# Optimization experiments

Hardware: AMD Instinct MI355X
Metric: run time of the kernel (lower is better)

## Reference

```python
import jax, jax.numpy as jnp
import numpy as np

N = 100000
E = 600000
NODE_DIM = 128
EDGE_DIM = 32
HIDDEN = 128  # must equal NODE_DIM (index_add_ into zeros_like(node_features))


def _linear_params(key, fan_in, fan_out):
    kw, kb = jax.random.split(key)
    bound = 1.0 / np.sqrt(fan_in)
    W = jax.random.uniform(kw, (fan_in, fan_out), minval=-bound, maxval=bound, dtype=jnp.float32)
    b = jax.random.uniform(kb, (fan_out,), minval=-bound, maxval=bound, dtype=jnp.float32)
    return W, b


def setup_inputs() -> dict:
    key = jax.random.key(0)
    ks = jax.random.split(key, 8)
    node_features = jax.random.normal(ks[0], (N, NODE_DIM), dtype=jnp.float32)
    edge_index = jax.random.randint(ks[1], (2, E), 0, N, dtype=jnp.int32)
    edge_features = jax.random.normal(ks[2], (E, EDGE_DIM), dtype=jnp.float32)
    m_W1, m_b1 = _linear_params(ks[3], 2 * NODE_DIM + EDGE_DIM, HIDDEN)
    m_W2, m_b2 = _linear_params(ks[4], HIDDEN, HIDDEN)
    a_W, a_b = _linear_params(ks[5], HIDDEN, 1)
    u_W1, u_b1 = _linear_params(ks[6], NODE_DIM + HIDDEN, HIDDEN)
    u_W2, u_b2 = _linear_params(ks[7], HIDDEN, NODE_DIM)
    return {
        "node_features": node_features,
        "edge_features": edge_features,
        "m_W1": m_W1, "m_b1": m_b1, "m_W2": m_W2, "m_b2": m_b2,
        "a_W": a_W, "a_b": a_b,
        "u_W1": u_W1, "u_b1": u_b1, "u_W2": u_W2, "u_b2": u_b2,
        "edge_index": edge_index,
    }


def reference(node_features, edge_features, m_W1, m_b1, m_W2, m_b2,
              a_W, a_b, u_W1, u_b1, u_W2, u_b2, edge_index):
    row, col = edge_index[0], edge_index[1]
    # gather endpoints + edge feats -> [E, 2*node_dim + edge_dim]
    msg_in = jnp.concatenate([node_features[row], node_features[col], edge_features], axis=-1)
    # message MLP
    h = jax.nn.relu(msg_in @ m_W1 + m_b1)
    messages = h @ m_W2 + m_b2  # [E, hidden]
    # global softmax over all edges (dim=0), per attention column (width 1)
    attn = jax.nn.softmax(messages @ a_W + a_b, axis=0)  # [E, 1]
    messages = messages * attn
    # scatter-add into destination nodes
    aggregated = jax.ops.segment_sum(messages, col, num_segments=node_features.shape[0])
    # update MLP + residual
    upd_in = jnp.concatenate([node_features, aggregated], axis=-1)
    u = jax.nn.relu(upd_in @ u_W1 + u_b1)
    updated = u @ u_W2 + u_b2
    return updated + node_features
```

## Files before the change

### kernel.cpp

```cpp
#include <hip/hip_runtime.h>
#include <hip/hip_bf16.h>
#include <stdint.h>

#define NN 100000
#define NE 600000
#define ND 128
#define ED 32
#define HID 128
#define SCANB 391

using short8 = __attribute__((ext_vector_type(8))) short;
using f32x4  = __attribute__((ext_vector_type(4))) float;

__device__ __forceinline__ uint32_t f2bf(float f) {
  uint32_t u = __float_as_uint(f);
  return (u + 0x7FFFu + ((u >> 16) & 1u)) >> 16;
}
__device__ __forceinline__ short8 pack8(float4 a, float4 b) {
  short8 s;
  s[0] = (short)f2bf(a.x); s[1] = (short)f2bf(a.y);
  s[2] = (short)f2bf(a.z); s[3] = (short)f2bf(a.w);
  s[4] = (short)f2bf(b.x); s[5] = (short)f2bf(b.y);
  s[6] = (short)f2bf(b.z); s[7] = (short)f2bf(b.w);
  return s;
}

__global__ __launch_bounds__(256) void k_prep(
    const float* __restrict__ W1, const float* __restrict__ W2,
    const float* __restrict__ uW1, const float* __restrict__ uW2,
    short* __restrict__ W1p, short* __restrict__ W2p,
    short* __restrict__ U1p, short* __restrict__ U2p) {
  int o = blockIdx.x * 256 + threadIdx.x;
  const float* src; short* dst; int rel;
  if (o < 36864)      { rel = o;         src = W1;  dst = W1p; }
  else if (o < 53248) { rel = o - 36864; src = W2;  dst = W2p; }
  else if (o < 86016) { rel = o - 53248; src = uW1; dst = U1p; }
  else                { rel = o - 86016; src = uW2; dst = U2p; }
  int j = rel & 7, c16 = (rel >> 3) & 15, g = (rel >> 7) & 3, nt = (rel >> 9) & 7, c = rel >> 12;
  int k = c * 32 + g * 8 + j, n = nt * 16 + c16;
  dst[rel] = (short)f2bf(src[k * 128 + n]);
}

__global__ __launch_bounds__(256) void k_prep_nf(const float* __restrict__ nf,
                                                 short* __restrict__ nfb) {
  const int total = NN * ND / 8;
  for (int u = blockIdx.x * 256 + threadIdx.x; u < total; u += gridDim.x * 256) {
    const float* s = nf + (size_t)u * 8;
    float4 v0 = *(const float4*)s, v1 = *(const float4*)(s + 4);
    *(short8*)(nfb + (size_t)u * 8) = pack8(v0, v1);
  }
}

__global__ __launch_bounds__(256, 2) void k_edge_mfma(
    const short* __restrict__ nfb, const float* __restrict__ ef,
    const short* __restrict__ W1p, const float* __restrict__ b1,
    const short* __restrict__ W2p, const float* __restrict__ b2,
    const float* __restrict__ aW, const int* __restrict__ ei,
    const int* __restrict__ perm,
    uint16_t* __restrict__ msg, float* __restrict__ logits) {
  __shared__ __align__(16) short sA[192 * 40];
  __shared__ __align__(16) short sB[4096];
  __shared__ __align__(16) short sH[192 * 136];
  __shared__ int sIdx[384];
  __shared__ int sPerm[192];

  const int tid = threadIdx.x;
  const int wv = tid >> 6, ln = tid & 63, cr = ln & 15, gp = ln >> 4;
  const int e0 = blockIdx.x * 192;
  const int wrow = wv * 48;

  if (tid < 192) {
    sIdx[tid] = ei[e0 + tid];
    sIdx[192 + tid] = ei[NE + e0 + tid];
    sPerm[tid] = perm[e0 + tid];
  }

  float bia[8], aWr[8], bia2[8];
#pragma unroll
  for (int nt = 0; nt < 8; ++nt) {
    bia[nt] = b1[nt * 16 + cr];
    bia2[nt] = b2[nt * 16 + cr];
    aWr[nt] = aW[nt * 16 + cr];
  }
  f32x4 acc[3][8];
#pragma unroll
  for (int mt = 0; mt < 3; ++mt)
#pragma unroll
    for (int nt = 0; nt < 8; ++nt)
      acc[mt][nt] = (f32x4){bia[nt], bia[nt], bia[nt], bia[nt]};
  __syncthreads();

  for (int c = 0; c < 9; ++c) {
#pragma unroll
    for (int it = 0; it < 3; ++it) {
      int row = it * 64 + (tid >> 2), k8 = (tid & 3) * 8;
      if (c < 8) {
        const short* src = nfb + (size_t)sIdx[(c < 4 ? 0 : 192) + row] * ND +
                           (c & 3) * 32 + k8;
        *(short8*)&sA[row * 40 + k8] = *(const short8*)src;
      } else {
        const float* src = ef + (size_t)(e0 + row) * ED + k8;
        float4 v0 = *(const float4*)src, v1 = *(const float4*)(src + 4);
        *(short8*)&sA[row * 40 + k8] = pack8(v0, v1);
      }
    }
    {
      const short8* wsrc = (const short8*)(W1p + c * 4096);
      short8 t0 = wsrc[tid], t1 = wsrc[tid + 256];
      ((short8*)sB)[tid] = t0; ((short8*)sB)[tid + 256] = t1;
    }
    __syncthreads();
    short8 af[3];
#pragma unroll
    for (int mt = 0; mt < 3; ++mt)
      af[mt] = *(const short8*)&sA[(wrow + mt * 16 + cr) * 40 + gp * 8];
#pragma unroll
    for (int nt = 0; nt < 8; ++nt) {
      short8 bfr = *(const short8*)&sB[(nt * 4 + gp) * 128 + cr * 8];
#pragma unroll
      for (int mt = 0; mt < 3; ++mt)
        acc[mt][nt] = __builtin_amdgcn_mfma_f32_16x16x32_bf16(af[mt], bfr, acc[mt][nt], 0, 0, 0);
    }
    __syncthreads();
  }

#pragma unroll
  for (int mt = 0; mt < 3; ++mt)
#pragma unroll
    for (int nt = 0; nt < 8; ++nt)
#pragma unroll
      for (int rr = 0; rr < 4; ++rr)
        sH[(wrow + mt * 16 + gp * 4 + rr) * 136 + nt * 16 + cr] =
            (short)f2bf(fmaxf(acc[mt][nt][rr], 0.f));
  __syncthreads();

  f32x4 acc2[3][8];
#pragma unroll
  for (int mt = 0; mt < 3; ++mt)
#pragma unroll
    for (int nt = 0; nt < 8; ++nt)
      acc2[mt][nt] = (f32x4){bia2[nt], bia2[nt], bia2[nt], bia2[nt]};
  for (int c2 = 0; c2 < 4; ++c2) {
    {
      const short8* wsrc = (const short8*)(W2p + c2 * 4096);
      short8 t0 = wsrc[tid], t1 = wsrc[tid + 256];
      ((short8*)sB)[tid] = t0; ((short8*)sB)[tid + 256] = t1;
    }
    __syncthreads();
    short8 af[3];
#pragma unroll
    for (int mt = 0; mt < 3; ++mt)
      af[mt] = *(const short8*)&sH[(wrow + mt * 16 + cr) * 136 + c2 * 32 + gp * 8];
#pragma unroll
    for (int nt = 0; nt < 8; ++nt) {
      short8 bfr = *(const short8*)&sB[(nt * 4 + gp) * 128 + cr * 8];
#pragma unroll
      for (int mt = 0; mt < 3; ++mt)
        acc2[mt][nt] = __builtin_amdgcn_mfma_f32_16x16x32_bf16(af[mt], bfr, acc2[mt][nt], 0, 0, 0);
    }
    __syncthreads();
  }

#pragma unroll
  for (int mt = 0; mt < 3; ++mt)
#pragma unroll
    for (int rr = 0; rr < 4; ++rr) {
      float p = 0.f;
#pragma unroll
      for (int nt = 0; nt < 8; ++nt) p += acc2[mt][nt][rr] * aWr[nt];
      p += __shfl_xor(p, 1, 64);
      p += __shfl_xor(p, 2, 64);
      p += __shfl_xor(p, 4, 64);
      p += __shfl_xor(p, 8, 64);
      if (cr == 0) logits[sPerm[wrow + mt * 16 + gp * 4 + rr]] = p;
    }

#pragma unroll
  for (int mt = 0; mt < 3; ++mt)
#pragma unroll
    for (int nt = 0; nt < 8; ++nt)
#pragma unroll
      for (int rr = 0; rr < 4; ++rr)
        sH[(wrow + mt * 16 + gp * 4 + rr) * 136 + nt * 16 + cr] =
            (short)f2bf(acc2[mt][nt][rr]);
  __syncthreads();
#pragma unroll
  for (int it = 0; it < 12; ++it) {
    int row = it * 16 + (tid >> 4), o8 = (tid & 15) * 8;
    *(short8*)(msg + (size_t)sPerm[row] * HID + o8) = *(const short8*)&sH[row * 136 + o8];
  }
}

__global__ __launch_bounds__(256, 2) void k_node_mfma(
    const float* __restrict__ nf, const short* __restrict__ nfb,
    const float* __restrict__ agg,
    const short* __restrict__ U1p, const float* __restrict__ b1,
    const short* __restrict__ U2p, const float* __restrict__ b2,
    float* __restrict__ out) {
  __shared__ __align__(16) short sA[192 * 40];
  __shared__ __align__(16) short sB[4096];
  __shared__ __align__(16) short sH[192 * 136];

  const int tid = threadIdx.x;
  const int wv = tid >> 6, ln = tid & 63, cr = ln & 15, gp = ln >> 4;
  const int n0 = blockIdx.x * 192;
  const int wrow = wv * 48;

  float bia[8], bia2[8];
#pragma unroll
  for (int nt = 0; nt < 8; ++nt) {
    bia[nt] = b1[nt * 16 + cr];
    bia2[nt] = b2[nt * 16 + cr];
  }
  f32x4 acc[3][8];
#pragma unroll
  for (int mt = 0; mt < 3; ++mt)
#pragma unroll
    for (int nt = 0; nt < 8; ++nt)
      acc[mt][nt] = (f32x4){bia[nt], bia[nt], bia[nt], bia[nt]};

  for (int c = 0; c < 8; ++c) {
#pragma unroll
    for (int it = 0; it < 3; ++it) {
      int row = it * 64 + (tid >> 2), k8 = (tid & 3) * 8;
      int n = n0 + row; if (n >= NN) n = NN - 1;
      if (c < 4) {
        *(short8*)&sA[row * 40 + k8] =
            *(const short8*)(nfb + (size_t)n * ND + c * 32 + k8);
      } else {
        const float* src = agg + (size_t)n * ND + (c - 4) * 32 + k8;
        float4 v0 = *(const float4*)src, v1 = *(const float4*)(src + 4);
        *(short8*)&sA[row * 40 + k8] = pack8(v0, v1);
      }
    }
    {
      const short8* wsrc = (const short8*)(U1p + c * 4096);
      short8 t0 = wsrc[tid], t1 = wsrc[tid + 256];
      ((short8*)sB)[tid] = t0; ((short8*)sB)[tid + 256] = t1;
    }
    __syncthreads();
    short8 af[3];
#pragma unroll
    for (int mt = 0; mt < 3; ++mt)
      af[mt] = *(const short8*)&sA[(wrow + mt * 16 + cr) * 40 + gp * 8];
#pragma unroll
    for (int nt = 0; nt < 8; ++nt) {
      short8 bfr = *(const short8*)&sB[(nt * 4 + gp) * 128 + cr * 8];
#pragma unroll
      for (int mt = 0; mt < 3; ++mt)
        acc[mt][nt] = __builtin_amdgcn_mfma_f32_16x16x32_bf16(af[mt], bfr, acc[mt][nt], 0, 0, 0);
    }
    __syncthreads();
  }

#pragma unroll
  for (int mt = 0; mt < 3; ++mt)
#pragma unroll
    for (int nt = 0; nt < 8; ++nt)
#pragma unroll
      for (int rr = 0; rr < 4; ++rr)
        sH[(wrow + mt * 16 + gp * 4 + rr) * 136 + nt * 16 + cr] =
            (short)f2bf(fmaxf(acc[mt][nt][rr], 0.f));
  __syncthreads();

  f32x4 acc2[3][8];
#pragma unroll
  for (int mt = 0; mt < 3; ++mt)
#pragma unroll
    for (int nt = 0; nt < 8; ++nt)
      acc2[mt][nt] = (f32x4){bia2[nt], bia2[nt], bia2[nt], bia2[nt]};
  for (int c2 = 0; c2 < 4; ++c2) {
    {
      const short8* wsrc = (const short8*)(U2p + c2 * 4096);
      short8 t0 = wsrc[tid], t1 = wsrc[tid + 256];
      ((short8*)sB)[tid] = t0; ((short8*)sB)[tid + 256] = t1;
    }
    __syncthreads();
    short8 af[3];
#pragma unroll
    for (int mt = 0; mt < 3; ++mt)
      af[mt] = *(const short8*)&sH[(wrow + mt * 16 + cr) * 136 + c2 * 32 + gp * 8];
#pragma unroll
    for (int nt = 0; nt < 8; ++nt) {
      short8 bfr = *(const short8*)&sB[(nt * 4 + gp) * 128 + cr * 8];
#pragma unroll
      for (int mt = 0; mt < 3; ++mt)
        acc2[mt][nt] = __builtin_amdgcn_mfma_f32_16x16x32_bf16(af[mt], bfr, acc2[mt][nt], 0, 0, 0);
    }
    __syncthreads();
  }

#pragma unroll
  for (int mt = 0; mt < 3; ++mt)
#pragma unroll
    for (int rr = 0; rr < 4; ++rr) {
      int n = n0 + wrow + mt * 16 + gp * 4 + rr;
      if (n < NN) {
#pragma unroll
        for (int nt = 0; nt < 8; ++nt) {
          int col = nt * 16 + cr;
          out[(size_t)n * ND + col] = acc2[mt][nt][rr] + nf[(size_t)n * ND + col];
        }
      }
    }
}

__device__ __forceinline__ void ms_combine(float& m, float& s, float m2, float s2) {
  float M = fmaxf(m, m2);
  s = s * expf(m - M) + s2 * expf(m2 - M);
  m = M;
}
__device__ __forceinline__ void ms_block_reduce(float& m, float& s) {
#pragma unroll
  for (int o = 1; o < 64; o <<= 1) {
    float m2 = __shfl_xor(m, o, 64), s2 = __shfl_xor(s, o, 64);
    ms_combine(m, s, m2, s2);
  }
  __shared__ float sm[4], ss[4];
  if ((threadIdx.x & 63) == 0) { sm[threadIdx.x >> 6] = m; ss[threadIdx.x >> 6] = s; }
  __syncthreads();
  m = sm[0]; s = ss[0];
  ms_combine(m, s, sm[1], ss[1]);
  ms_combine(m, s, sm[2], ss[2]);
  ms_combine(m, s, sm[3], ss[3]);
}
__global__ __launch_bounds__(256) void k_red_p(const float* __restrict__ logits,
                                               float* __restrict__ pmax,
                                               float* __restrict__ psum) {
  float m = -3.402823466e38f, s = 0.f;
  for (int i = blockIdx.x * 256 + threadIdx.x; i < NE; i += 1024 * 256) {
    float l = logits[i];
    if (l <= m) s += expf(l - m);
    else { s = s * expf(m - l) + 1.f; m = l; }
  }
  ms_block_reduce(m, s);
  if (threadIdx.x == 0) { pmax[blockIdx.x] = m; psum[blockIdx.x] = s; }
}
__global__ __launch_bounds__(256) void k_red_f(const float* __restrict__ pmax,
                                               const float* __restrict__ psum,
                                               float* __restrict__ red) {
  float m = pmax[threadIdx.x], s = psum[threadIdx.x];
  ms_combine(m, s, pmax[threadIdx.x + 256], psum[threadIdx.x + 256]);
  ms_combine(m, s, pmax[threadIdx.x + 512], psum[threadIdx.x + 512]);
  ms_combine(m, s, pmax[threadIdx.x + 768], psum[threadIdx.x + 768]);
  ms_block_reduce(m, s);
  if (threadIdx.x == 0) { red[0] = m; red[1] = 1.0f / s; }
}

__global__ __launch_bounds__(256) void k_zero_cnt(int* __restrict__ cnt) {
  int i = blockIdx.x * 256 + threadIdx.x;
  if (i < NN) cnt[i] = 0;
}
__global__ __launch_bounds__(256) void k_hist(const int* __restrict__ ei,
                                              int* __restrict__ cnt) {
  int e = blockIdx.x * 256 + threadIdx.x;
  if (e < NE) atomicAdd(&cnt[ei[NE + e]], 1);
}
__global__ __launch_bounds__(256) void k_scan_bsum(const int* __restrict__ cnt,
                                                   int* __restrict__ bsum) {
  int i = blockIdx.x * 256 + threadIdx.x;
  int v = (i < NN) ? cnt[i] : 0;
#pragma unroll
  for (int s = 1; s < 64; s <<= 1) v += __shfl_xor(v, s, 64);
  __shared__ int sv[4];
  if ((threadIdx.x & 63) == 0) sv[threadIdx.x >> 6] = v;
  __syncthreads();
  if (threadIdx.x == 0) bsum[blockIdx.x] = sv[0] + sv[1] + sv[2] + sv[3];
}
__global__ __launch_bounds__(512) void k_scan_boff(const int* __restrict__ bsum,
                                                   int* __restrict__ boff,
                                                   int* __restrict__ rowptr) {
  __shared__ int s[512];
  int t = threadIdx.x;
  int v = (t < SCANB) ? bsum[t] : 0;
  s[t] = v;
  __syncthreads();
  for (int off = 1; off < 512; off <<= 1) {
    int u = (t >= off) ? s[t - off] : 0;
    __syncthreads();
    s[t] += u;
    __syncthreads();
  }
  if (t < SCANB) boff[t] = s[t] - v;
  if (t == 0) rowptr[NN] = NE;
}
__global__ __launch_bounds__(256) void k_scan_final(int* __restrict__ cnt,
                                                    const int* __restrict__ boff,
                                                    int* __restrict__ rowptr) {
  __shared__ int s[256];
  int b = blockIdx.x, t = threadIdx.x, i = b * 256 + t;
  int v = (i < NN) ? cnt[i] : 0;
  s[t] = v;
  __syncthreads();
  for (int off = 1; off < 256; off <<= 1) {
    int u = (t >= off) ? s[t - off] : 0;
    __syncthreads();
    s[t] += u;
    __syncthreads();
  }
  int excl = s[t] - v + boff[b];
  if (i < NN) { rowptr[i] = excl; cnt[i] = excl; }
}
__global__ __launch_bounds__(256) void k_fill(const int* __restrict__ ei,
                                              int* __restrict__ cursor,
                                              int* __restrict__ perm) {
  int e = blockIdx.x * 256 + threadIdx.x;
  if (e >= NE) return;
  int c = ei[NE + e];
  int pos = atomicAdd(&cursor[c], 1);
  perm[e] = pos;
}

__global__ __launch_bounds__(256) void k_agg(
    const uint16_t* __restrict__ msg, const float* __restrict__ logits,
    const int* __restrict__ rowptr, const float* __restrict__ red,
    float* __restrict__ out) {
  int n = blockIdx.x * 4 + (threadIdx.x >> 6);
  int lane = threadIdx.x & 63;
  if (n >= NN) return;
  float gm = red[0], inv = red[1];
  int i0 = rowptr[n], i1 = rowptr[n + 1];
  float a0 = 0.f, a1 = 0.f;
  for (int i = i0; i < i1; ++i) {
    float wt = expf(logits[i] - gm) * inv;
    uint32_t pk = *(const uint32_t*)(msg + (size_t)i * HID + lane * 2);
    a0 += wt * __uint_as_float(pk << 16);
    a1 += wt * __uint_as_float(pk & 0xFFFF0000u);
  }
  *(float2*)(out + (size_t)n * ND + lane * 2) = make_float2(a0, a1);
}

extern "C" void kernel_launch(void* const* d_in, const int* in_sizes, int n_in,
                              void* d_out, int out_size, void* d_ws, size_t ws_size,
                              hipStream_t stream) {
  const float* nf  = (const float*)d_in[0];
  const float* ef  = (const float*)d_in[1];
  const float* mW1 = (const float*)d_in[2];
  const float* mb1 = (const float*)d_in[3];
  const float* mW2 = (const float*)d_in[4];
  const float* mb2 = (const float*)d_in[5];
  const float* aW  = (const float*)d_in[6];
  const float* uW1 = (const float*)d_in[8];
  const float* ub1 = (const float*)d_in[9];
  const float* uW2 = (const float*)d_in[10];
  const float* ub2 = (const float*)d_in[11];
  const int*   ei  = (const int*)d_in[12];
  float* out = (float*)d_out;

  char* ws = (char*)d_ws;
  uint16_t* msg = (uint16_t*)ws;
  float* logits = (float*)(ws + 153600000);
  float* pmax = (float*)(ws + 156000000);
  float* psum = pmax + 1024;
  float* red  = psum + 1024;
  short* W1p = (short*)(ws + 156008256);
  short* W2p = W1p + 36864;
  short* U1p = W2p + 16384;
  short* U2p = U1p + 32768;
  int* rowptr = (int*)(ws + 156213056);
  int* cnt    = rowptr + (NN + 1);
  int* perm   = cnt + NN;
  int* bsum   = perm + NE;
  int* boff   = bsum + 512;
  short* nfb  = (short*)(ws + 159420416);

  k_prep<<<400, 256, 0, stream>>>(mW1, mW2, uW1, uW2, W1p, W2p, U1p, U2p);
  k_prep_nf<<<2048, 256, 0, stream>>>(nf, nfb);
  k_zero_cnt<<<SCANB, 256, 0, stream>>>(cnt);
  k_hist<<<(NE + 255) / 256, 256, 0, stream>>>(ei, cnt);
  k_scan_bsum<<<SCANB, 256, 0, stream>>>(cnt, bsum);
  k_scan_boff<<<1, 512, 0, stream>>>(bsum, boff, rowptr);
  k_scan_final<<<SCANB, 256, 0, stream>>>(cnt, boff, rowptr);
  k_fill<<<(NE + 255) / 256, 256, 0, stream>>>(ei, cnt, perm);
  k_edge_mfma<<<NE / 192, 256, 0, stream>>>(nfb, ef, W1p, mb1, W2p, mb2, aW, ei, perm, msg, logits);
  k_red_p<<<1024, 256, 0, stream>>>(logits, pmax, psum);
  k_red_f<<<1, 256, 0, stream>>>(pmax, psum, red);
  k_agg<<<(NN + 3) / 4, 256, 0, stream>>>(msg, logits, rowptr, red, out);
  k_node_mfma<<<(NN + 191) / 192, 256, 0, stream>>>(nf, nfb, out, U1p, ub1, U2p, ub2, out);
}
```

Baseline: 361.6 us.

## Process edges in sorted order and fuse softmax partial reduction into edge kernel

Result: slower. 386.4 us (+6.9%).

```diff
diff --git a/kernel.cpp b/kernel.cpp
--- a/kernel.cpp
+++ b/kernel.cpp
@@ -8,6 +8,7 @@
 #define ED 32
 #define HID 128
 #define SCANB 391
+#define NB (NE / 192)
 
 using short8 = __attribute__((ext_vector_type(8))) short;
 using f32x4  = __attribute__((ext_vector_type(4))) float;
@@ -23,6 +24,26 @@
   s[4] = (short)f2bf(b.x); s[5] = (short)f2bf(b.y);
   s[6] = (short)f2bf(b.z); s[7] = (short)f2bf(b.w);
   return s;
+}
+
+__device__ __forceinline__ void ms_combine(float& m, float& s, float m2, float s2) {
+  float M = fmaxf(m, m2);
+  s = s * expf(m - M) + s2 * expf(m2 - M);
+  m = M;
+}
+__device__ __forceinline__ void ms_block_reduce(float& m, float& s) {
+#pragma unroll
+  for (int o = 1; o < 64; o <<= 1) {
+    float m2 = __shfl_xor(m, o, 64), s2 = __shfl_xor(s, o, 64);
+    ms_combine(m, s, m2, s2);
+  }
+  __shared__ float sm[4], ss[4];
+  if ((threadIdx.x & 63) == 0) { sm[threadIdx.x >> 6] = m; ss[threadIdx.x >> 6] = s; }
+  __syncthreads();
+  m = sm[0]; s = ss[0];
+  ms_combine(m, s, sm[1], ss[1]);
+  ms_combine(m, s, sm[2], ss[2]);
+  ms_combine(m, s, sm[3], ss[3]);
 }
 
 __global__ __launch_bounds__(256) void k_prep(
@@ -56,13 +77,14 @@
     const short* __restrict__ W1p, const float* __restrict__ b1,
     const short* __restrict__ W2p, const float* __restrict__ b2,
     const float* __restrict__ aW, const int* __restrict__ ei,
-    const int* __restrict__ perm,
-    uint16_t* __restrict__ msg, float* __restrict__ logits) {
+    const int* __restrict__ eid,
+    uint16_t* __restrict__ msg, float* __restrict__ logits,
+    float* __restrict__ pmaxp, float* __restrict__ psump) {
   __shared__ __align__(16) short sA[192 * 40];
   __shared__ __align__(16) short sB[4096];
   __shared__ __align__(16) short sH[192 * 136];
   __shared__ int sIdx[384];
-  __shared__ int sPerm[192];
+  __shared__ int sEid[192];
 
   const int tid = threadIdx.x;
   const int wv = tid >> 6, ln = tid & 63, cr = ln & 15, gp = ln >> 4;
@@ -70,9 +92,10 @@
   const int wrow = wv * 48;
 
   if (tid < 192) {
-    sIdx[tid] = ei[e0 + tid];
-    sIdx[192 + tid] = ei[NE + e0 + tid];
-    sPerm[tid] = perm[e0 + tid];
+    int e = eid[e0 + tid];
+    sEid[tid] = e;
+    sIdx[tid] = ei[e];
+    sIdx[192 + tid] = ei[NE + e];
   }
 
   float bia[8], aWr[8], bia2[8];
@@ -99,7 +122,7 @@
                            (c & 3) * 32 + k8;
         *(short8*)&sA[row * 40 + k8] = *(const short8*)src;
       } else {
-        const float* src = ef + (size_t)(e0 + row) * ED + k8;
+        const float* src = ef + (size_t)sEid[row] * ED + k8;
         float4 v0 = *(const float4*)src, v1 = *(const float4*)(src + 4);
         *(short8*)&sA[row * 40 + k8] = pack8(v0, v1);
       }
@@ -161,6 +184,7 @@
     __syncthreads();
   }
 
+  float pm = -3.402823466e38f, ps = 0.f;
 #pragma unroll
   for (int mt = 0; mt < 3; ++mt)
 #pragma unroll
@@ -172,8 +196,14 @@
       p += __shfl_xor(p, 2, 64);
       p += __shfl_xor(p, 4, 64);
       p += __shfl_xor(p, 8, 64);
-      if (cr == 0) logits[sPerm[wrow + mt * 16 + gp * 4 + rr]] = p;
-    }
+      if (cr == 0) {
+        logits[e0 + wrow + mt * 16 + gp * 4 + rr] = p;
+        if (p <= pm) ps += expf(p - pm);
+        else { ps = ps * expf(pm - p) + 1.f; pm = p; }
+      }
+    }
+  ms_block_reduce(pm, ps);
+  if (tid == 0) { pmaxp[blockIdx.x] = pm; psump[blockIdx.x] = ps; }
 
 #pragma unroll
   for (int mt = 0; mt < 3; ++mt)
@@ -187,7 +217,7 @@
 #pragma unroll
   for (int it = 0; it < 12; ++it) {
     int row = it * 16 + (tid >> 4), o8 = (tid & 15) * 8;
-    *(short8*)(msg + (size_t)sPerm[row] * HID + o8) = *(const short8*)&sH[row * 136 + o8];
+    *(short8*)(msg + (size_t)(e0 + row) * HID + o8) = *(const short8*)&sH[row * 136 + o8];
   }
 }
 
@@ -305,44 +335,11 @@
     }
 }
 
-__device__ __forceinline__ void ms_combine(float& m, float& s, float m2, float s2) {
-  float M = fmaxf(m, m2);
-  s = s * expf(m - M) + s2 * expf(m2 - M);
-  m = M;
-}
-__device__ __forceinline__ void ms_block_reduce(float& m, float& s) {
-#pragma unroll
-  for (int o = 1; o < 64; o <<= 1) {
-    float m2 = __shfl_xor(m, o, 64), s2 = __shfl_xor(s, o, 64);
-    ms_combine(m, s, m2, s2);
-  }
-  __shared__ float sm[4], ss[4];
-  if ((threadIdx.x & 63) == 0) { sm[threadIdx.x >> 6] = m; ss[threadIdx.x >> 6] = s; }
-  __syncthreads();
-  m = sm[0]; s = ss[0];
-  ms_combine(m, s, sm[1], ss[1]);
-  ms_combine(m, s, sm[2], ss[2]);
-  ms_combine(m, s, sm[3], ss[3]);
-}
-__global__ __launch_bounds__(256) void k_red_p(const float* __restrict__ logits,
-                                               float* __restrict__ pmax,
-                                               float* __restrict__ psum) {
+__global__ __launch_bounds__(256) void k_red_f(const float* __restrict__ pmaxp,
+                                               const float* __restrict__ psump,
+                                               float* __restrict__ red) {
   float m = -3.402823466e38f, s = 0.f;
-  for (int i = blockIdx.x * 256 + threadIdx.x; i < NE; i += 1024 * 256) {
-    float l = logits[i];
-    if (l <= m) s += expf(l - m);
-    else { s = s * expf(m - l) + 1.f; m = l; }
-  }
-  ms_block_reduce(m, s);
-  if (threadIdx.x == 0) { pmax[blockIdx.x] = m; psum[blockIdx.x] = s; }
-}
-__global__ __launch_bounds__(256) void k_red_f(const float* __restrict__ pmax,
-                                               const float* __restrict__ psum,
-                                               float* __restrict__ red) {
-  float m = pmax[threadIdx.x], s = psum[threadIdx.x];
-  ms_combine(m, s, pmax[threadIdx.x + 256], psum[threadIdx.x + 256]);
-  ms_combine(m, s, pmax[threadIdx.x + 512], psum[threadIdx.x + 512]);
-  ms_combine(m, s, pmax[threadIdx.x + 768], psum[threadIdx.x + 768]);
+  for (int i = threadIdx.x; i < NB; i += 256) ms_combine(m, s, pmaxp[i], psump[i]);
   ms_block_reduce(m, s);
   if (threadIdx.x == 0) { red[0] = m; red[1] = 1.0f / s; }
 }
@@ -403,12 +400,12 @@
 }
 __global__ __launch_bounds__(256) void k_fill(const int* __restrict__ ei,
                                               int* __restrict__ cursor,
-                                              int* __restrict__ perm) {
+                                              int* __restrict__ eid) {
   int e = blockIdx.x * 256 + threadIdx.x;
   if (e >= NE) return;
   int c = ei[NE + e];
   int pos = atomicAdd(&cursor[c], 1);
-  perm[e] = pos;
+  eid[pos] = e;
 }
 
 __global__ __launch_bounds__(256) void k_agg(
@@ -450,19 +447,19 @@
   char* ws = (char*)d_ws;
   uint16_t* msg = (uint16_t*)ws;
   float* logits = (float*)(ws + 153600000);
-  float* pmax = (float*)(ws + 156000000);
-  float* psum = pmax + 1024;
-  float* red  = psum + 1024;
-  short* W1p = (short*)(ws + 156008256);
+  short* W1p = (short*)(ws + 156000000);
   short* W2p = W1p + 36864;
   short* U1p = W2p + 16384;
   short* U2p = U1p + 32768;
-  int* rowptr = (int*)(ws + 156213056);
+  int* rowptr = (int*)(ws + 156204800);
   int* cnt    = rowptr + (NN + 1);
-  int* perm   = cnt + NN;
-  int* bsum   = perm + NE;
+  int* eid    = cnt + NN;
+  int* bsum   = eid + NE;
   int* boff   = bsum + 512;
-  short* nfb  = (short*)(ws + 159420416);
+  short* nfb  = (short*)(ws + 159408912);
+  float* pmaxp = (float*)(ws + 185008912);
+  float* psump = pmaxp + 3200;
+  float* red   = psump + 3200;
 
   k_prep<<<400, 256, 0, stream>>>(mW1, mW2, uW1, uW2, W1p, W2p, U1p, U2p);
   k_prep_nf<<<2048, 256, 0, stream>>>(nf, nfb);
@@ -471,10 +468,10 @@
   k_scan_bsum<<<SCANB, 256, 0, stream>>>(cnt, bsum);
   k_scan_boff<<<1, 512, 0, stream>>>(bsum, boff, rowptr);
   k_scan_final<<<SCANB, 256, 0, stream>>>(cnt, boff, rowptr);
-  k_fill<<<(NE + 255) / 256, 256, 0, stream>>>(ei, cnt, perm);
-  k_edge_mfma<<<NE / 192, 256, 0, stream>>>(nfb, ef, W1p, mb1, W2p, mb2, aW, ei, perm, msg, logits);
-  k_red_p<<<1024, 256, 0, stream>>>(logits, pmax, psum);
-  k_red_f<<<1, 256, 0, stream>>>(pmax, psum, red);
+  k_fill<<<(NE + 255) / 256, 256, 0, stream>>>(ei, cnt, eid);
+  k_edge_mfma<<<NB, 256, 0, stream>>>(nfb, ef, W1p, mb1, W2p, mb2, aW, ei, eid,
+                                      msg, logits, pmaxp, psump);
+  k_red_f<<<1, 256, 0, stream>>>(pmaxp, psump, red);
   k_agg<<<(NN + 3) / 4, 256, 0, stream>>>(msg, logits, rowptr, red, out);
   k_node_mfma<<<(NN + 191) / 192, 256, 0, stream>>>(nf, nfb, out, U1p, ub1, U2p, ub2, out);
 }
```
